# Kernel optimization log

Hardware: AMD Instinct MI355X
Metric: run time of the kernel (lower is better)

Reference implementation:

```python
import jax, jax.numpy as jnp
import numpy as np

B, S, D = 2, 2048, 512
H = 8
G = 4
LAMBDA_INIT = 0.2  # 0.8 - 0.6*exp(-0.3*(layer_idx-1)) with layer_idx=1
EPS = 1e-5


def setup_inputs() -> dict:
    key = jax.random.key(0)
    ks = jax.random.split(key, 16)
    n = jax.random.normal
    return {
        "x": n(ks[0], (B, S, D), jnp.float32),
        "K1_w": n(ks[1], (D, D), jnp.float32) * 0.02,
        "K1_b": n(ks[2], (D,), jnp.float32) * 0.02,
        "Q1_w": n(ks[3], (D, D), jnp.float32) * 0.02,
        "K2_w": n(ks[4], (D, D), jnp.float32) * 0.02,
        "K2_b": n(ks[5], (D,), jnp.float32) * 0.02,
        "Q2_w": n(ks[6], (D, D), jnp.float32) * 0.02,
        "V_w": n(ks[7], (D, D), jnp.float32) * 0.02,
        "lambda_q1": n(ks[8], (H, 1), jnp.float32),
        "lambda_k1": n(ks[9], (H, 1), jnp.float32),
        "lambda_q2": n(ks[10], (H, 1), jnp.float32),
        "lambda_k2": n(ks[11], (H, 1), jnp.float32),
        "gn_w": jnp.ones((D,), jnp.float32),
        "gn_b": jnp.zeros((D,), jnp.float32),
        "out_w": n(ks[12], (D, D), jnp.float32) * 0.02,
        "out_b": n(ks[13], (D,), jnp.float32) * 0.02,
    }


def reference(x, K1_w, K1_b, Q1_w, K2_w, K2_b, Q2_w, V_w,
              lambda_q1, lambda_k1, lambda_q2, lambda_k2,
              gn_w, gn_b, out_w, out_b):
    b, s, d = x.shape
    hd = d // H

    def heads(t):  # (b,s,d) -> (b,H,s,hd)
        return t.reshape(b, s, H, hd).transpose(0, 2, 1, 3)

    q1 = heads(x @ Q1_w.T)
    k1 = heads(x @ K1_w.T + K1_b)
    q2 = heads(x @ Q2_w.T)
    k2 = heads(x @ K2_w.T + K2_b)
    v = heads(x @ V_w.T)

    scale = hd ** 0.5
    a1 = jax.nn.softmax(jnp.einsum('bhqd,bhkd->bhqk', q1, k1) / scale, axis=-1)
    a2 = jax.nn.softmax(jnp.einsum('bhqd,bhkd->bhqk', q2, k2) / scale, axis=-1)

    lam = (jnp.exp(lambda_q1 * lambda_k1)
           - jnp.exp(lambda_q2 * lambda_k2) + LAMBDA_INIT)  # (H,1)
    attn = a1 - lam.reshape(1, H, 1, 1) * a2

    o = jnp.einsum('bhqk,bhkd->bhqd', attn, v)
    o = o.transpose(0, 2, 1, 3).reshape(b, s, d)

    # GroupNorm over channels: input (b, d, s), groups G normalize over (d/G, s)
    xc = o.transpose(0, 2, 1).reshape(b, G, d // G, s)
    mu = xc.mean(axis=(2, 3), keepdims=True)
    var = xc.var(axis=(2, 3), keepdims=True)
    xn = ((xc - mu) * jax.lax.rsqrt(var + EPS)).reshape(b, d, s)
    xn = xn * gn_w[None, :, None] + gn_b[None, :, None]

    y = xn.transpose(0, 2, 1) @ out_w.T + out_b
    return y
```

## Files before the change

kernel.cpp:

```cpp
#include <hip/hip_runtime.h>
#include <hip/hip_bf16.h>

typedef __bf16 bf16;
typedef __attribute__((ext_vector_type(8))) __bf16 bf16x8;
typedef __attribute__((ext_vector_type(4))) float f32x4;

#define MFMA16(a, b, c) __builtin_amdgcn_mfma_f32_16x16x32_bf16((a), (b), (c), 0, 0, 0)

static constexpr float EPS = 1e-5f;
static constexpr float LAMBDA_INIT = 0.2f;

__device__ __forceinline__ bf16x8 cvt8(const float* p) {
    const f32x4 a = *(const f32x4*)p;
    const f32x4 b = *(const f32x4*)(p + 4);
    bf16x8 r;
    r[0] = (bf16)a[0]; r[1] = (bf16)a[1]; r[2] = (bf16)a[2]; r[3] = (bf16)a[3];
    r[4] = (bf16)b[0]; r[5] = (bf16)b[1]; r[6] = (bf16)b[2]; r[7] = (bf16)b[3];
    return r;
}

__device__ __forceinline__ void gload_lds16(const void* g, void* l) {
    __builtin_amdgcn_global_load_lds(
        (const __attribute__((address_space(1))) unsigned int*)g,
        (__attribute__((address_space(3))) unsigned int*)l,
        16, 0, 0);
}

__global__ __launch_bounds__(256) void prep_kernel(
    const float* __restrict__ x,
    const float* __restrict__ q1w, const float* __restrict__ k1w,
    const float* __restrict__ q2w, const float* __restrict__ k2w,
    const float* __restrict__ vw,
    const float* __restrict__ ow, const float* __restrict__ gnw,
    const float* __restrict__ gnb,
    bf16* __restrict__ xb, bf16* __restrict__ wb,
    bf16* __restrict__ owg, float* __restrict__ S0, float* __restrict__ stats)
{
    const int tid = threadIdx.x;
    if (blockIdx.x < 1664) {
        const size_t base = ((size_t)blockIdx.x * 256 + tid) * 8;
        if (base < 2097152) {
            *(bf16x8*)(xb + base) = cvt8(x + base);
        } else {
            const size_t wbase = base - 2097152;
            const int wsel = (int)(wbase >> 18);
            const size_t off = wbase & 262143;
            const float* W = (wsel == 0) ? q1w : (wsel == 1) ? k1w :
                             (wsel == 2) ? q2w : (wsel == 3) ? k2w : vw;
            *(bf16x8*)(wb + wbase) = cvt8(W + off);
        }
        return;
    }

    __shared__ float red[4];
    const int pb = blockIdx.x - 1664;
    if (pb == 0 && tid < 16) stats[tid] = 0.f;

    const int n0 = pb * 16;
    const int c0 = tid, c1 = tid + 256;
    const float gw0 = gnw[c0], gw1 = gnw[c1];
    const float gb0 = gnb[c0], gb1 = gnb[c1];

    for (int n = 0; n < 16; ++n) {
        const size_t rowb = (size_t)(n0 + n) * 512;
        const float w0 = ow[rowb + c0];
        const float w1 = ow[rowb + c1];
        owg[rowb + c0] = (bf16)(w0 * gw0);
        owg[rowb + c1] = (bf16)(w1 * gw1);
        float s = gb0 * w0 + gb1 * w1;
#pragma unroll
        for (int off = 1; off < 64; off <<= 1) s += __shfl_xor(s, off, 64);
        if ((tid & 63) == 0) red[tid >> 6] = s;
        __syncthreads();
        if (tid == 0) S0[n0 + n] = red[0] + red[1] + red[2] + red[3];
        __syncthreads();
    }
}

__global__ __launch_bounds__(256) void proj_kernel(
    const bf16* __restrict__ xb, const bf16* __restrict__ wb,
    const float* __restrict__ k1b, const float* __restrict__ k2b,
    bf16* __restrict__ q1o, bf16* __restrict__ k1o,
    bf16* __restrict__ q2o, bf16* __restrict__ k2o,
    bf16* __restrict__ vto)
{
    __shared__ __align__(16) bf16 As[128 * 32];
    __shared__ __align__(16) bf16 Bs[128 * 32];

    const int tid = threadIdx.x;
    const int wave = tid >> 6, lane = tid & 63;
    const int l15 = lane & 15, quad = lane >> 4;
    const int wm = wave >> 1, wn = wave & 1;

    const int mb = blockIdx.x / 20;
    const int nb = blockIdx.x % 20;
    const int wsel = nb >> 2;
    const int nrow0 = (nb & 3) * 128;

    const int srow = lane >> 2;
    const int scol = (lane & 3) * 8;
    const bf16* ag = xb + (size_t)(mb * 128 + srow) * 512 + scol;
    const bf16* bg = wb + (size_t)(wsel * 512 + nrow0 + srow) * 512 + scol;

    f32x4 acc[4][4];
#pragma unroll
    for (int i = 0; i < 4; ++i)
#pragma unroll
        for (int j = 0; j < 4; ++j)
            acc[i][j] = (f32x4){0.f, 0.f, 0.f, 0.f};

    for (int k0 = 0; k0 < 512; k0 += 32) {
#pragma unroll
        for (int c = 0; c < 2; ++c) {
            const int chunk = wave * 2 + c;
            gload_lds16(ag + (size_t)(chunk * 16) * 512 + k0, As + chunk * 512);
            gload_lds16(bg + (size_t)(chunk * 16) * 512 + k0, Bs + chunk * 512);
        }
        __syncthreads();

        bf16x8 af[4], bfr[4];
#pragma unroll
        for (int i = 0; i < 4; ++i)
            af[i] = *(const bf16x8*)(As + (wm * 64 + i * 16 + l15) * 32 + quad * 8);
#pragma unroll
        for (int j = 0; j < 4; ++j)
            bfr[j] = *(const bf16x8*)(Bs + (wn * 64 + j * 16 + l15) * 32 + quad * 8);

#pragma unroll
        for (int i = 0; i < 4; ++i)
#pragma unroll
            for (int j = 0; j < 4; ++j)
                acc[i][j] = MFMA16(af[i], bfr[j], acc[i][j]);

        __syncthreads();
    }

    const float scale = (wsel == 0 || wsel == 2) ? 0.125f : 1.0f;
#pragma unroll
    for (int j = 0; j < 4; ++j) {
        const int ncol = nrow0 + wn * 64 + j * 16 + l15;
        float bias = 0.f;
        if (wsel == 1) bias = k1b[ncol];
        if (wsel == 3) bias = k2b[ncol];
        const int h = ncol >> 6, hd = ncol & 63;
#pragma unroll
        for (int i = 0; i < 4; ++i) {
#pragma unroll
            for (int r = 0; r < 4; ++r) {
                const int m = mb * 128 + wm * 64 + i * 16 + quad * 4 + r;
                const int bidx = m >> 11, s = m & 2047;
                const float v = acc[i][j][r] * scale + bias;
                if (wsel == 4) {
                    const int s5 = s & 31;
                    const int p = ((s5 & 15) >> 2) * 8 + (s5 & 3) + ((s5 >> 4) << 2);
                    const int sp = (s & ~31) | p;
                    vto[((size_t)(bidx * 8 + h) * 64 + hd) * 2048 + sp] = (bf16)v;
                } else {
                    bf16* dst = (wsel == 0) ? q1o : (wsel == 1) ? k1o :
                                (wsel == 2) ? q2o : k2o;
                    dst[((size_t)(bidx * 8 + h) * 2048 + s) * 64 + hd] = (bf16)v;
                }
            }
        }
    }
}

__global__ __launch_bounds__(512, 4) void attn_kernel(
    const bf16* __restrict__ q1, const bf16* __restrict__ k1,
    const bf16* __restrict__ q2, const bf16* __restrict__ k2,
    const bf16* __restrict__ vt,
    const float* __restrict__ lq1, const float* __restrict__ lk1,
    const float* __restrict__ lq2, const float* __restrict__ lk2,
    bf16* __restrict__ o, float* __restrict__ stats)
{
    __shared__ __align__(16) bf16 smem[12288];
    __shared__ float lbuf[8][2][16];
    __shared__ float sred[8][2];

    const int tid = threadIdx.x;
    const int wave = tid >> 6;
    const int lane = tid & 63;
    const int l15 = lane & 15, quad = lane >> 4;
    const int qtile = wave & 3;
    const int kg = wave >> 2;

    const int bh = blockIdx.x >> 5;
    const int qt = blockIdx.x & 31;
    const int b = bh >> 3, h = bh & 7;

    const bf16* k1t = k1 + (size_t)bh * 2048 * 64;
    const bf16* k2t = k2 + (size_t)bh * 2048 * 64;
    const bf16* vtt = vt + (size_t)bh * 64 * 2048;

    const int qrow = qt * 64 + qtile * 16 + l15;
    const bf16* q1p = q1 + ((size_t)bh * 2048 + qrow) * 64 + quad * 8;
    const bf16* q2p = q2 + ((size_t)bh * 2048 + qrow) * 64 + quad * 8;
    const bf16x8 q1f0 = *(const bf16x8*)(q1p);
    const bf16x8 q1f1 = *(const bf16x8*)(q1p + 32);
    const bf16x8 q2f0 = *(const bf16x8*)(q2p);
    const bf16x8 q2f1 = *(const bf16x8*)(q2p + 32);

    const int sw = wave & 3;
    const int skey0 = (wave < 4) ? 0 : 1024;
    bf16* k1dst = smem + wave * 512;
    bf16* k2dst = smem + 4096 + wave * 512;
    bf16* vdst  = smem + 8192 + wave * 512;
    const size_t ksrc0 = (size_t)(skey0 + sw * 8 + (lane >> 3)) * 64
                       + 8 * ((lane & 7) ^ (lane >> 3));
    const size_t vsrc0 = (size_t)(sw * 16 + (lane >> 2)) * 2048 + skey0 + (lane & 3) * 8;

    const bf16* k1r = smem + kg * 2048;
    const bf16* k2r = smem + 4096 + kg * 2048;
    const bf16* vr  = smem + 8192 + kg * 2048;

    const int koffa = 8 * (quad ^ (l15 & 7));
    const int koffb = 8 * ((quad + 4) ^ (l15 & 7));

    f32x4 O1[4], O2[4];
    float l1 = 0.f, l2 = 0.f;
#pragma unroll
    for (int t = 0; t < 4; ++t) {
        O1[t] = (f32x4){0.f, 0.f, 0.f, 0.f};
        O2[t] = (f32x4){0.f, 0.f, 0.f, 0.f};
    }

    for (int it = 0; it < 32; ++it) {
        const size_t koff = ksrc0 + (size_t)it * 32 * 64;
        gload_lds16(k1t + koff, k1dst);
        gload_lds16(k2t + koff, k2dst);
        gload_lds16(vtt + vsrc0 + it * 32, vdst);
        __syncthreads();

        const bf16x8 k1t0a = *(const bf16x8*)(k1r + l15 * 64 + koffa);
        const bf16x8 k1t0b = *(const bf16x8*)(k1r + l15 * 64 + koffb);
        const bf16x8 k1t1a = *(const bf16x8*)(k1r + (16 + l15) * 64 + koffa);
        const bf16x8 k1t1b = *(const bf16x8*)(k1r + (16 + l15) * 64 + koffb);
        const bf16x8 k2t0a = *(const bf16x8*)(k2r + l15 * 64 + koffa);
        const bf16x8 k2t0b = *(const bf16x8*)(k2r + l15 * 64 + koffb);
        const bf16x8 k2t1a = *(const bf16x8*)(k2r + (16 + l15) * 64 + koffa);
        const bf16x8 k2t1b = *(const bf16x8*)(k2r + (16 + l15) * 64 + koffb);
        const bf16x8 v0 = *(const bf16x8*)(vr + l15 * 32 + quad * 8);
        const bf16x8 v1 = *(const bf16x8*)(vr + (16 + l15) * 32 + quad * 8);
        const bf16x8 v2 = *(const bf16x8*)(vr + (32 + l15) * 32 + quad * 8);
        const bf16x8 v3 = *(const bf16x8*)(vr + (48 + l15) * 32 + quad * 8);

        f32x4 z = (f32x4){0.f, 0.f, 0.f, 0.f};
        f32x4 s1t0 = MFMA16(k1t0a, q1f0, z);  s1t0 = MFMA16(k1t0b, q1f1, s1t0);
        f32x4 s1t1 = MFMA16(k1t1a, q1f0, z);  s1t1 = MFMA16(k1t1b, q1f1, s1t1);
        f32x4 s2t0 = MFMA16(k2t0a, q2f0, z);  s2t0 = MFMA16(k2t0b, q2f1, s2t0);
        f32x4 s2t1 = MFMA16(k2t1a, q2f0, z);  s2t1 = MFMA16(k2t1b, q2f1, s2t1);

        bf16x8 b1, b2;
#pragma unroll
        for (int r = 0; r < 4; ++r) {
            float e;
            e = __expf(s1t0[r]); l1 += e; b1[r]     = (bf16)e;
            e = __expf(s1t1[r]); l1 += e; b1[4 + r] = (bf16)e;
            e = __expf(s2t0[r]); l2 += e; b2[r]     = (bf16)e;
            e = __expf(s2t1[r]); l2 += e; b2[4 + r] = (bf16)e;
        }

        O1[0] = MFMA16(v0, b1, O1[0]);
        O1[1] = MFMA16(v1, b1, O1[1]);
        O1[2] = MFMA16(v2, b1, O1[2]);
        O1[3] = MFMA16(v3, b1, O1[3]);
        O2[0] = MFMA16(v0, b2, O2[0]);
        O2[1] = MFMA16(v1, b2, O2[1]);
        O2[2] = MFMA16(v2, b2, O2[2]);
        O2[3] = MFMA16(v3, b2, O2[3]);

        __syncthreads();
    }

    l1 += __shfl_xor(l1, 16, 64);  l1 += __shfl_xor(l1, 32, 64);
    l2 += __shfl_xor(l2, 16, 64);  l2 += __shfl_xor(l2, 32, 64);
    if (lane < 16) {
        lbuf[wave][0][lane] = l1;
        lbuf[wave][1][lane] = l2;
    }
    __syncthreads();

    f32x4* rb = (f32x4*)smem;
    if (wave == 4 || wave == 5) {
        f32x4* dst = rb + (wave - 4) * 512;
#pragma unroll
        for (int t = 0; t < 4; ++t) {
            dst[t * 64 + lane]       = O1[t];
            dst[(4 + t) * 64 + lane] = O2[t];
        }
    }
    __syncthreads();
    if (wave == 0 || wave == 1) {
        const f32x4* src = rb + wave * 512;
#pragma unroll
        for (int t = 0; t < 4; ++t) {
            O1[t] += src[t * 64 + lane];
            O2[t] += src[(4 + t) * 64 + lane];
        }
    }
    __syncthreads();
    if (wave == 6 || wave == 7) {
        f32x4* dst = rb + (wave - 6) * 512;
#pragma unroll
        for (int t = 0; t < 4; ++t) {
            dst[t * 64 + lane]       = O1[t];
            dst[(4 + t) * 64 + lane] = O2[t];
        }
    }
    __syncthreads();
    if (wave == 2 || wave == 3) {
        const f32x4* src = rb + (wave - 2) * 512;
#pragma unroll
        for (int t = 0; t < 4; ++t) {
            O1[t] += src[t * 64 + lane];
            O2[t] += src[(4 + t) * 64 + lane];
        }
    }

    float ssum = 0.f, ssq = 0.f;
    if (wave < 4) {
        const float L1 = l1 + lbuf[wave + 4][0][l15];
        const float L2 = l2 + lbuf[wave + 4][1][l15];
        const float lam = __expf(lq1[h] * lk1[h]) - __expf(lq2[h] * lk2[h]) + LAMBDA_INIT;
        const float inv1 = 1.f / L1;
        const float inv2 = lam / L2;
        const size_t row = (size_t)(b * 2048 + qt * 64 + wave * 16 + l15) * 512 + h * 64;
#pragma unroll
        for (int t = 0; t < 4; ++t) {
#pragma unroll
            for (int r = 0; r < 4; ++r) {
                const float val = O1[t][r] * inv1 - O2[t][r] * inv2;
                ssum += val;
                ssq += val * val;
                o[row + t * 16 + quad * 4 + r] = (bf16)val;
            }
        }
    }
#pragma unroll
    for (int off = 1; off < 64; off <<= 1) {
        ssum += __shfl_xor(ssum, off, 64);
        ssq += __shfl_xor(ssq, off, 64);
    }
    if (lane == 0) { sred[wave][0] = ssum; sred[wave][1] = ssq; }
    __syncthreads();
    if (tid == 0) {
        float s0 = 0.f, s1 = 0.f;
        for (int w = 0; w < 8; ++w) { s0 += sred[w][0]; s1 += sred[w][1]; }
        const int bg = b * 4 + (h >> 1);
        atomicAdd(&stats[bg * 2], s0);
        atomicAdd(&stats[bg * 2 + 1], s1);
    }
}

__global__ __launch_bounds__(256) void out_gemm_kernel(
    const bf16* __restrict__ o, const bf16* __restrict__ owg,
    const float* __restrict__ S0, const float* __restrict__ stats,
    const float* __restrict__ ob, float* __restrict__ y)
{
    __shared__ __align__(16) bf16 As[64 * 32];
    __shared__ __align__(16) bf16 Bs[64 * 32];

    const int tid = threadIdx.x;
    const int wave = tid >> 6, lane = tid & 63;
    const int l15 = lane & 15, quad = lane >> 4;

    const int mb = blockIdx.x >> 3;
    const int nb = blockIdx.x & 7;
    const int b = mb >> 5;

    const float N = 128.f * 2048.f;
    float mu[4], rs[4];
#pragma unroll
    for (int g = 0; g < 4; ++g) {
        const float m = stats[(b * 4 + g) * 2] / N;
        const float var = stats[(b * 4 + g) * 2 + 1] / N - m * m;
        mu[g] = m;
        rs[g] = rsqrtf(var + EPS);
    }

    const int srow = wave * 16 + (lane >> 2);
    const int scol = (lane & 3) * 8;
    const bf16* ag = o + (size_t)(mb * 64 + srow) * 512 + scol;
    const bf16* bg = owg + (size_t)(nb * 64 + srow) * 512 + scol;
    bf16* adst = As + wave * 512;
    bf16* bdst = Bs + wave * 512;

    f32x4 acc[4], tot[4];
#pragma unroll
    for (int i = 0; i < 4; ++i) {
        acc[i] = (f32x4){0.f, 0.f, 0.f, 0.f};
        tot[i] = (f32x4){0.f, 0.f, 0.f, 0.f};
    }
    float s1g[4];
    float s1p = 0.f;
#pragma unroll
    for (int g = 0; g < 4; ++g) s1g[g] = 0.f;

    for (int kk = 0; kk < 16; ++kk) {
        gload_lds16(ag + kk * 32, adst);
        gload_lds16(bg + kk * 32, bdst);
        __syncthreads();

        bf16x8 af[4];
#pragma unroll
        for (int i = 0; i < 4; ++i)
            af[i] = *(const bf16x8*)(As + (i * 16 + l15) * 32 + quad * 8);
        const bf16x8 bf = *(const bf16x8*)(Bs + (wave * 16 + l15) * 32 + quad * 8);

#pragma unroll
        for (int i = 0; i < 4; ++i)
            acc[i] = MFMA16(af[i], bf, acc[i]);

#pragma unroll
        for (int j = 0; j < 8; ++j) s1p += (float)bf[j];

        __syncthreads();

        if ((kk & 3) == 3) {
            const int g = kk >> 2;
#pragma unroll
            for (int i = 0; i < 4; ++i) {
#pragma unroll
                for (int r = 0; r < 4; ++r) tot[i][r] += rs[g] * acc[i][r];
                acc[i] = (f32x4){0.f, 0.f, 0.f, 0.f};
            }
            float sg = s1p + __shfl_xor(s1p, 16, 64);
            sg += __shfl_xor(sg, 32, 64);
            s1g[g] = sg;
            s1p = 0.f;
        }
    }

    const int ncol = nb * 64 + wave * 16 + l15;
    float bias = S0[ncol] + ob[ncol];
#pragma unroll
    for (int g = 0; g < 4; ++g) bias -= mu[g] * rs[g] * s1g[g];

#pragma unroll
    for (int i = 0; i < 4; ++i) {
#pragma unroll
        for (int r = 0; r < 4; ++r) {
            const int m = mb * 64 + i * 16 + quad * 4 + r;
            y[(size_t)m * 512 + ncol] = tot[i][r] + bias;
        }
    }
}

extern "C" void kernel_launch(void* const* d_in, const int* in_sizes, int n_in,
                              void* d_out, int out_size, void* d_ws, size_t ws_size,
                              hipStream_t stream)
{
    const float* x   = (const float*)d_in[0];
    const float* K1w = (const float*)d_in[1];
    const float* K1b = (const float*)d_in[2];
    const float* Q1w = (const float*)d_in[3];
    const float* K2w = (const float*)d_in[4];
    const float* K2b = (const float*)d_in[5];
    const float* Q2w = (const float*)d_in[6];
    const float* Vw  = (const float*)d_in[7];
    const float* lq1 = (const float*)d_in[8];
    const float* lk1 = (const float*)d_in[9];
    const float* lq2 = (const float*)d_in[10];
    const float* lk2 = (const float*)d_in[11];
    const float* gnw = (const float*)d_in[12];
    const float* gnb = (const float*)d_in[13];
    const float* Ow  = (const float*)d_in[14];
    const float* Ob  = (const float*)d_in[15];

    const size_t SZ = (size_t)2 * 8 * 2048 * 64;
    bf16* q1 = (bf16*)d_ws;
    bf16* k1 = q1 + SZ;
    bf16* q2 = k1 + SZ;
    bf16* k2 = q2 + SZ;
    bf16* vt = k2 + SZ;
    bf16* o  = vt + SZ;
    bf16* xb = o;
    bf16* wb = o + SZ;
    bf16* owg = wb + (size_t)2560 * 512;
    float* S0 = (float*)(owg + 512 * 512);
    float* stats = S0 + 512;

    prep_kernel<<<1696, 256, 0, stream>>>(x, Q1w, K1w, Q2w, K2w, Vw,
                                          Ow, gnw, gnb, xb, wb, owg, S0, stats);
    proj_kernel<<<640, 256, 0, stream>>>(xb, wb, K1b, K2b,
                                         q1, k1, q2, k2, vt);
    attn_kernel<<<512, 512, 0, stream>>>(q1, k1, q2, k2, vt,
                                         lq1, lk1, lq2, lk2, o, stats);
    out_gemm_kernel<<<512, 256, 0, stream>>>(o, owg, S0, stats, Ob,
                                             (float*)d_out);
}
```

Before: 188.3 us.

## Double-buffer LDS loads, use exp2 with folded log2e, swizzle V layout

Adds double-buffered global-to-LDS prefetch in the projection, attention and output GEMM kernels so loads for the next tile overlap compute on the current one. Folds log2(e) into the Q scaling so the softmax can use the hardware exp2 instruction. Swizzles the transposed V layout to reduce LDS bank conflicts, and remaps block indices in attention. Doubling LDS use in attention may reduce occupancy, and correctness relies on the barrier waiting for the asynchronous LDS loads.

```diff
diff --git a/kernel.cpp b/kernel.cpp
--- a/kernel.cpp
+++ b/kernel.cpp
@@ -9,6 +9,7 @@
 
 static constexpr float EPS = 1e-5f;
 static constexpr float LAMBDA_INIT = 0.2f;
+static constexpr float LOG2E = 1.44269504088896340736f;
 
 __device__ __forceinline__ bf16x8 cvt8(const float* p) {
     const f32x4 a = *(const f32x4*)p;
@@ -84,8 +85,8 @@
     bf16* __restrict__ q2o, bf16* __restrict__ k2o,
     bf16* __restrict__ vto)
 {
-    __shared__ __align__(16) bf16 As[128 * 32];
-    __shared__ __align__(16) bf16 Bs[128 * 32];
+    __shared__ __align__(16) bf16 As[2][128 * 32];
+    __shared__ __align__(16) bf16 Bs[2][128 * 32];
 
     const int tid = threadIdx.x;
     const int wave = tid >> 6, lane = tid & 63;
@@ -109,22 +110,35 @@
         for (int j = 0; j < 4; ++j)
             acc[i][j] = (f32x4){0.f, 0.f, 0.f, 0.f};
 
-    for (int k0 = 0; k0 < 512; k0 += 32) {
-#pragma unroll
-        for (int c = 0; c < 2; ++c) {
-            const int chunk = wave * 2 + c;
-            gload_lds16(ag + (size_t)(chunk * 16) * 512 + k0, As + chunk * 512);
-            gload_lds16(bg + (size_t)(chunk * 16) * 512 + k0, Bs + chunk * 512);
-        }
-        __syncthreads();
-
+#pragma unroll
+    for (int c = 0; c < 2; ++c) {
+        const int chunk = wave * 2 + c;
+        gload_lds16(ag + (size_t)(chunk * 16) * 512, As[0] + chunk * 512);
+        gload_lds16(bg + (size_t)(chunk * 16) * 512, Bs[0] + chunk * 512);
+    }
+    __syncthreads();
+
+    for (int s = 0; s < 16; ++s) {
+        const int cur = s & 1;
+        if (s < 15) {
+            const int k0n = (s + 1) * 32;
+#pragma unroll
+            for (int c = 0; c < 2; ++c) {
+                const int chunk = wave * 2 + c;
+                gload_lds16(ag + (size_t)(chunk * 16) * 512 + k0n, As[cur ^ 1] + chunk * 512);
+                gload_lds16(bg + (size_t)(chunk * 16) * 512 + k0n, Bs[cur ^ 1] + chunk * 512);
+            }
+        }
+
+        const bf16* Ac = As[cur];
+        const bf16* Bc = Bs[cur];
         bf16x8 af[4], bfr[4];
 #pragma unroll
         for (int i = 0; i < 4; ++i)
-            af[i] = *(const bf16x8*)(As + (wm * 64 + i * 16 + l15) * 32 + quad * 8);
+            af[i] = *(const bf16x8*)(Ac + (wm * 64 + i * 16 + l15) * 32 + quad * 8);
 #pragma unroll
         for (int j = 0; j < 4; ++j)
-            bfr[j] = *(const bf16x8*)(Bs + (wn * 64 + j * 16 + l15) * 32 + quad * 8);
+            bfr[j] = *(const bf16x8*)(Bc + (wn * 64 + j * 16 + l15) * 32 + quad * 8);
 
 #pragma unroll
         for (int i = 0; i < 4; ++i)
@@ -135,7 +149,7 @@
         __syncthreads();
     }
 
-    const float scale = (wsel == 0 || wsel == 2) ? 0.125f : 1.0f;
+    const float scale = (wsel == 0 || wsel == 2) ? 0.125f * LOG2E : 1.0f;
 #pragma unroll
     for (int j = 0; j < 4; ++j) {
         const int ncol = nrow0 + wn * 64 + j * 16 + l15;
@@ -143,6 +157,7 @@
         if (wsel == 1) bias = k1b[ncol];
         if (wsel == 3) bias = k2b[ncol];
         const int h = ncol >> 6, hd = ncol & 63;
+        const int xh = (hd >> 1) & 3;
 #pragma unroll
         for (int i = 0; i < 4; ++i) {
 #pragma unroll
@@ -152,7 +167,9 @@
                 const float v = acc[i][j][r] * scale + bias;
                 if (wsel == 4) {
                     const int s5 = s & 31;
-                    const int p = ((s5 & 15) >> 2) * 8 + (s5 & 3) + ((s5 >> 4) << 2);
+                    const int q = (s5 >> 2) & 3;
+                    const int jj = (s5 & 3) + ((s5 >> 4) << 2);
+                    const int p = ((q ^ xh) << 3) | jj;
                     const int sp = (s & ~31) | p;
                     vto[((size_t)(bidx * 8 + h) * 64 + hd) * 2048 + sp] = (bf16)v;
                 } else {
@@ -173,7 +190,7 @@
     const float* __restrict__ lq2, const float* __restrict__ lk2,
     bf16* __restrict__ o, float* __restrict__ stats)
 {
-    __shared__ __align__(16) bf16 smem[12288];
+    __shared__ __align__(16) bf16 smem[2][12288];
     __shared__ float lbuf[8][2][16];
     __shared__ float sred[8][2];
 
@@ -184,8 +201,9 @@
     const int qtile = wave & 3;
     const int kg = wave >> 2;
 
-    const int bh = blockIdx.x >> 5;
-    const int qt = blockIdx.x & 31;
+    const int rid = (blockIdx.x & 7) * 64 + (blockIdx.x >> 3);
+    const int bh = rid >> 5;
+    const int qt = rid & 31;
     const int b = bh >> 3, h = bh & 7;
 
     const bf16* k1t = k1 + (size_t)bh * 2048 * 64;
@@ -202,19 +220,13 @@
 
     const int sw = wave & 3;
     const int skey0 = (wave < 4) ? 0 : 1024;
-    bf16* k1dst = smem + wave * 512;
-    bf16* k2dst = smem + 4096 + wave * 512;
-    bf16* vdst  = smem + 8192 + wave * 512;
     const size_t ksrc0 = (size_t)(skey0 + sw * 8 + (lane >> 3)) * 64
                        + 8 * ((lane & 7) ^ (lane >> 3));
     const size_t vsrc0 = (size_t)(sw * 16 + (lane >> 2)) * 2048 + skey0 + (lane & 3) * 8;
 
-    const bf16* k1r = smem + kg * 2048;
-    const bf16* k2r = smem + 4096 + kg * 2048;
-    const bf16* vr  = smem + 8192 + kg * 2048;
-
     const int koffa = 8 * (quad ^ (l15 & 7));
     const int koffb = 8 * ((quad + 4) ^ (l15 & 7));
+    const int vsw = 8 * (quad ^ ((l15 >> 1) & 3));
 
     f32x4 O1[4], O2[4];
     float l1 = 0.f, l2 = 0.f;
@@ -224,12 +236,26 @@
         O2[t] = (f32x4){0.f, 0.f, 0.f, 0.f};
     }
 
+    gload_lds16(k1t + ksrc0, smem[0] + wave * 512);
+    gload_lds16(k2t + ksrc0, smem[0] + 4096 + wave * 512);
+    gload_lds16(vtt + vsrc0, smem[0] + 8192 + wave * 512);
+    __syncthreads();
+
     for (int it = 0; it < 32; ++it) {
-        const size_t koff = ksrc0 + (size_t)it * 32 * 64;
-        gload_lds16(k1t + koff, k1dst);
-        gload_lds16(k2t + koff, k2dst);
-        gload_lds16(vtt + vsrc0 + it * 32, vdst);
-        __syncthreads();
+        const int cur = it & 1;
+        const bf16* sb = smem[cur];
+
+        if (it < 31) {
+            bf16* nb_ = smem[cur ^ 1];
+            const size_t koff = ksrc0 + (size_t)(it + 1) * 32 * 64;
+            gload_lds16(k1t + koff, nb_ + wave * 512);
+            gload_lds16(k2t + koff, nb_ + 4096 + wave * 512);
+            gload_lds16(vtt + vsrc0 + (it + 1) * 32, nb_ + 8192 + wave * 512);
+        }
+
+        const bf16* k1r = sb + kg * 2048;
+        const bf16* k2r = sb + 4096 + kg * 2048;
+        const bf16* vr  = sb + 8192 + kg * 2048;
 
         const bf16x8 k1t0a = *(const bf16x8*)(k1r + l15 * 64 + koffa);
         const bf16x8 k1t0b = *(const bf16x8*)(k1r + l15 * 64 + koffb);
@@ -239,10 +265,10 @@
         const bf16x8 k2t0b = *(const bf16x8*)(k2r + l15 * 64 + koffb);
         const bf16x8 k2t1a = *(const bf16x8*)(k2r + (16 + l15) * 64 + koffa);
         const bf16x8 k2t1b = *(const bf16x8*)(k2r + (16 + l15) * 64 + koffb);
-        const bf16x8 v0 = *(const bf16x8*)(vr + l15 * 32 + quad * 8);
-        const bf16x8 v1 = *(const bf16x8*)(vr + (16 + l15) * 32 + quad * 8);
-        const bf16x8 v2 = *(const bf16x8*)(vr + (32 + l15) * 32 + quad * 8);
-        const bf16x8 v3 = *(const bf16x8*)(vr + (48 + l15) * 32 + quad * 8);
+        const bf16x8 v0 = *(const bf16x8*)(vr + l15 * 32 + vsw);
+        const bf16x8 v1 = *(const bf16x8*)(vr + (16 + l15) * 32 + vsw);
+        const bf16x8 v2 = *(const bf16x8*)(vr + (32 + l15) * 32 + vsw);
+        const bf16x8 v3 = *(const bf16x8*)(vr + (48 + l15) * 32 + vsw);
 
         f32x4 z = (f32x4){0.f, 0.f, 0.f, 0.f};
         f32x4 s1t0 = MFMA16(k1t0a, q1f0, z);  s1t0 = MFMA16(k1t0b, q1f1, s1t0);
@@ -254,10 +280,10 @@
 #pragma unroll
         for (int r = 0; r < 4; ++r) {
             float e;
-            e = __expf(s1t0[r]); l1 += e; b1[r]     = (bf16)e;
-            e = __expf(s1t1[r]); l1 += e; b1[4 + r] = (bf16)e;
-            e = __expf(s2t0[r]); l2 += e; b2[r]     = (bf16)e;
-            e = __expf(s2t1[r]); l2 += e; b2[4 + r] = (bf16)e;
+            e = __builtin_amdgcn_exp2f(s1t0[r]); l1 += e; b1[r]     = (bf16)e;
+            e = __builtin_amdgcn_exp2f(s1t1[r]); l1 += e; b1[4 + r] = (bf16)e;
+            e = __builtin_amdgcn_exp2f(s2t0[r]); l2 += e; b2[r]     = (bf16)e;
+            e = __builtin_amdgcn_exp2f(s2t1[r]); l2 += e; b2[4 + r] = (bf16)e;
         }
 
         O1[0] = MFMA16(v0, b1, O1[0]);
@@ -357,8 +383,8 @@
     const float* __restrict__ S0, const float* __restrict__ stats,
     const float* __restrict__ ob, float* __restrict__ y)
 {
-    __shared__ __align__(16) bf16 As[64 * 32];
-    __shared__ __align__(16) bf16 Bs[64 * 32];
+    __shared__ __align__(16) bf16 As[2][64 * 32];
+    __shared__ __align__(16) bf16 Bs[2][64 * 32];
 
     const int tid = threadIdx.x;
     const int wave = tid >> 6, lane = tid & 63;
@@ -382,8 +408,6 @@
     const int scol = (lane & 3) * 8;
     const bf16* ag = o + (size_t)(mb * 64 + srow) * 512 + scol;
     const bf16* bg = owg + (size_t)(nb * 64 + srow) * 512 + scol;
-    bf16* adst = As + wave * 512;
-    bf16* bdst = Bs + wave * 512;
 
     f32x4 acc[4], tot[4];
 #pragma unroll
@@ -396,16 +420,22 @@
 #pragma unroll
     for (int g = 0; g < 4; ++g) s1g[g] = 0.f;
 
+    gload_lds16(ag, As[0] + wave * 512);
+    gload_lds16(bg, Bs[0] + wave * 512);
+    __syncthreads();
+
     for (int kk = 0; kk < 16; ++kk) {
-        gload_lds16(ag + kk * 32, adst);
-        gload_lds16(bg + kk * 32, bdst);
-        __syncthreads();
+        const int cur = kk & 1;
+        if (kk < 15) {
+            gload_lds16(ag + (kk + 1) * 32, As[cur ^ 1] + wave * 512);
+            gload_lds16(bg + (kk + 1) * 32, Bs[cur ^ 1] + wave * 512);
+        }
 
         bf16x8 af[4];
 #pragma unroll
         for (int i = 0; i < 4; ++i)
-            af[i] = *(const bf16x8*)(As + (i * 16 + l15) * 32 + quad * 8);
-        const bf16x8 bf = *(const bf16x8*)(Bs + (wave * 16 + l15) * 32 + quad * 8);
+            af[i] = *(const bf16x8*)(As[cur] + (i * 16 + l15) * 32 + quad * 8);
+        const bf16x8 bf = *(const bf16x8*)(Bs[cur] + (wave * 16 + l15) * 32 + quad * 8);
 
 #pragma unroll
         for (int i = 0; i < 4; ++i)
```

Result: faster. 181.7 us (-3.5%).
